# Kernel optimization log

Measured on AMD Instinct MI355X. Metric: run time of the kernel, lower is better.

Reference implementation:

```python
import jax, jax.numpy as jnp
import numpy as np

N_RES = 2_000_000
N_DOM = 2
B_WIN = 100
S_STRIDE = 10
HIDDEN = 128


def _build_windows():
    # Faithful port of the __init__ index construction.
    nb_per_res = B_WIN // S_STRIDE
    balance = B_WIN - S_STRIDE + 1
    start = np.maximum(np.arange(N_RES) + balance - B_WIN, 0)
    start = start // S_STRIDE + (start % S_STRIDE != 0).astype(np.int64)
    bs = start[:, None] + np.arange(nb_per_res)[None, :]
    return bs.astype(np.int32)


def setup_inputs() -> dict:
    key = jax.random.key(0)
    ks = jax.random.split(key, 7)
    bs_per_res = _build_windows()
    nb_windows = int(bs_per_res[-1, -1]) + 1  # 200009
    # weights near 1 (original inits to ones) so products stay well-scaled
    weights = jax.random.uniform(ks[0], (nb_windows, N_DOM), minval=0.5, maxval=1.5, dtype=jnp.float32)
    latent_variables = jax.random.normal(ks[1], (6,), dtype=jnp.float32)
    features = jax.random.normal(ks[2], (2, 50), dtype=jnp.float32)  # replaces torch.randn((2,50))
    W1 = jax.random.normal(ks[3], (53, HIDDEN), dtype=jnp.float32) * 0.1
    b1 = jnp.zeros((HIDDEN,), dtype=jnp.float32)
    W2 = jax.random.normal(ks[4], (HIDDEN, 3), dtype=jnp.float32) * 0.1
    b2 = jnp.zeros((3,), dtype=jnp.float32)
    local_frame = jax.random.normal(ks[5], (3, 3), dtype=jnp.float32)
    atom_absolute_positions = jax.random.normal(ks[6], (3 * N_RES, 3), dtype=jnp.float32)
    return {
        'weights': weights,
        'latent_variables': latent_variables,
        'features': features,
        'W1': W1, 'b1': b1, 'W2': W2, 'b2': b2,
        'local_frame': local_frame,
        'atom_absolute_positions': atom_absolute_positions,
        'bs_per_res': jnp.asarray(bs_per_res),
    }


def multiply_windows_weights(weights, bs_per_res):
    # gather: (N_res, nb_per_res, N_dom); product over the window axis, softmax over domains
    gathered = weights[bs_per_res]
    weights_per_residue = jnp.prod(gathered, axis=1)
    return jax.nn.softmax(weights_per_residue, axis=1)


def reference(weights, latent_variables, features, W1, b1, W2, b2,
              local_frame, atom_absolute_positions, bs_per_res):
    attn = multiply_windows_weights(weights, bs_per_res)  # (N_res, N_dom)
    # features_and_latent: (2, 53)
    fl = jnp.concatenate([features, latent_variables.reshape(2, 3)], axis=1)
    h = jax.nn.relu(fl @ W1 + b1)
    scalars_per_domain = h @ W2 + b2  # (N_dom, 3)
    # deform_structure: note module stores local_frame transposed
    translation_vectors = scalars_per_domain @ local_frame.T  # (N_dom, 3)
    translation_per_residue = attn @ translation_vectors      # (N_res, 3)
    new_atom_positions = atom_absolute_positions + jnp.repeat(translation_per_residue, 3, axis=0)
    return new_atom_positions, attn, translation_per_residue
```

## Files before the change

kernel.cpp:

```cpp
#include <hip/hip_runtime.h>

#define N_RES   2000000
#define HIDDEN  128

__global__ void mlp_kernel(const float* __restrict__ latent,
                           const float* __restrict__ features,
                           const float* __restrict__ W1,
                           const float* __restrict__ b1,
                           const float* __restrict__ W2,
                           const float* __restrict__ b2,
                           const float* __restrict__ lf,
                           float* __restrict__ tv_out)
{
    __shared__ float h[2][HIDDEN];
    __shared__ float s[2][3];
    const int tid = threadIdx.x;
    const int d = tid >> 7;
    const int j = tid & 127;

    float acc = b1[j];
    #pragma unroll 10
    for (int k = 0; k < 50; ++k)
        acc += features[d * 50 + k] * W1[k * HIDDEN + j];
    #pragma unroll
    for (int k = 0; k < 3; ++k)
        acc += latent[d * 3 + k] * W1[(50 + k) * HIDDEN + j];
    h[d][j] = fmaxf(acc, 0.0f);
    __syncthreads();

    if (tid < 6) {
        const int dd = tid / 3, c = tid % 3;
        float a = b2[c];
        #pragma unroll 16
        for (int k = 0; k < HIDDEN; ++k)
            a += h[dd][k] * W2[k * 3 + c];
        s[dd][c] = a;
    }
    __syncthreads();

    if (tid < 6) {
        const int dd = tid / 3, c = tid % 3;
        float a = 0.0f;
        #pragma unroll
        for (int k = 0; k < 3; ++k)
            a += s[dd][k] * lf[c * 3 + k];
        tv_out[dd * 3 + c] = a;
    }
}

__global__ void deform_kernel(const float* __restrict__ weights,
                              const float* __restrict__ pos,
                              const float* __restrict__ tv,
                              float* __restrict__ out_pos,
                              float* __restrict__ out_attn,
                              float* __restrict__ out_trans)
{
    const int r = blockIdx.x * blockDim.x + threadIdx.x;
    if (r >= N_RES) return;

    const int raw   = max(r - 9, 0);
    const int start = (raw + 9) / 10;

    const float2* wbase = (const float2*)(weights) + start;
    float p0 = 1.0f, p1 = 1.0f;
    #pragma unroll
    for (int j = 0; j < 10; ++j) {
        const float2 w = wbase[j];
        p0 *= w.x;
        p1 *= w.y;
    }

    const float m  = fmaxf(p0, p1);
    const float e0 = __expf(p0 - m);
    const float e1 = __expf(p1 - m);
    const float inv = 1.0f / (e0 + e1);
    const float a0 = e0 * inv;
    const float a1 = e1 * inv;

    ((float2*)out_attn)[r] = make_float2(a0, a1);

    const float t0 = a0 * tv[0] + a1 * tv[3];
    const float t1 = a0 * tv[1] + a1 * tv[4];
    const float t2 = a0 * tv[2] + a1 * tv[5];

    out_trans[3 * r + 0] = t0;
    out_trans[3 * r + 1] = t1;
    out_trans[3 * r + 2] = t2;

    const float* p = pos     + 9ll * r;
    float*       o = out_pos + 9ll * r;
    #pragma unroll
    for (int a = 0; a < 3; ++a) {
        o[3 * a + 0] = p[3 * a + 0] + t0;
        o[3 * a + 1] = p[3 * a + 1] + t1;
        o[3 * a + 2] = p[3 * a + 2] + t2;
    }
}

extern "C" void kernel_launch(void* const* d_in, const int* in_sizes, int n_in,
                              void* d_out, int out_size, void* d_ws, size_t ws_size,
                              hipStream_t stream) {
    const float* weights  = (const float*)d_in[0];
    const float* latent   = (const float*)d_in[1];
    const float* features = (const float*)d_in[2];
    const float* W1       = (const float*)d_in[3];
    const float* b1       = (const float*)d_in[4];
    const float* W2       = (const float*)d_in[5];
    const float* b2       = (const float*)d_in[6];
    const float* lf       = (const float*)d_in[7];
    const float* pos      = (const float*)d_in[8];

    float* out = (float*)d_out;
    float* tv  = (float*)d_ws;

    mlp_kernel<<<1, 256, 0, stream>>>(latent, features, W1, b1, W2, b2, lf, tv);

    const int blocks = (N_RES + 255) / 256;
    deform_kernel<<<blocks, 256, 0, stream>>>(
        weights, pos, tv,
        out,
        out + 18000000,
        out + 22000000);
}
```

Before: 233.7 us.

## Fuse MLP into deform kernel and coalesce position/translation I/O via LDS

Every block now recomputes the tiny MLP redundantly, which removes the separate single-block launch and the dependency between the two kernels. Position loads and stores, and the translation stores, are rewritten as block-cooperative float4 accesses, with per-residue translations staged in LDS, replacing the strided 9-float and 3-float per-thread accesses. The position loads are issued before the MLP so their latency overlaps it. In exchange, every block repeats the MLP's W1 reads and compute and adds several barriers.

```diff
diff --git a/kernel.cpp b/kernel.cpp
--- a/kernel.cpp
+++ b/kernel.cpp
@@ -2,99 +2,130 @@
 
 #define N_RES   2000000
 #define HIDDEN  128
+#define BLK     256
 
-__global__ void mlp_kernel(const float* __restrict__ latent,
-                           const float* __restrict__ features,
-                           const float* __restrict__ W1,
-                           const float* __restrict__ b1,
-                           const float* __restrict__ W2,
-                           const float* __restrict__ b2,
-                           const float* __restrict__ lf,
-                           float* __restrict__ tv_out)
+__global__ __launch_bounds__(BLK, 4) void fused_kernel(
+    const float* __restrict__ weights,
+    const float* __restrict__ latent,
+    const float* __restrict__ features,
+    const float* __restrict__ W1,
+    const float* __restrict__ b1,
+    const float* __restrict__ W2,
+    const float* __restrict__ b2,
+    const float* __restrict__ lf,
+    const float* __restrict__ pos,
+    float* __restrict__ out_pos,
+    float* __restrict__ out_attn,
+    float* __restrict__ out_trans)
 {
     __shared__ float h[2][HIDDEN];
-    __shared__ float s[2][3];
-    const int tid = threadIdx.x;
-    const int d = tid >> 7;
-    const int j = tid & 127;
+    __shared__ float sv[6];
+    __shared__ float tvs[6];
+    __shared__ __align__(16) float t_lds[3 * BLK];
 
-    float acc = b1[j];
-    #pragma unroll 10
-    for (int k = 0; k < 50; ++k)
-        acc += features[d * 50 + k] * W1[k * HIDDEN + j];
-    #pragma unroll
-    for (int k = 0; k < 3; ++k)
-        acc += latent[d * 3 + k] * W1[(50 + k) * HIDDEN + j];
-    h[d][j] = fmaxf(acc, 0.0f);
+    const int tid  = threadIdx.x;
+    const int r0   = blockIdx.x * BLK;
+    const int r    = r0 + tid;
+    const int nres = min(BLK, N_RES - r0);
+    const int nch  = (9 * nres) >> 2;
+
+    const float4* __restrict__ pos4 = (const float4*)(pos + 9ll * r0);
+    float4 pA = make_float4(0.f,0.f,0.f,0.f);
+    float4 pB = pA, pC = pA;
+    if (tid            < nch) pA = pos4[tid];
+    if (tid +     BLK  < nch) pB = pos4[tid + BLK];
+    if (tid + 2 * BLK  < nch) pC = pos4[tid + 2 * BLK];
+
+    {
+        const int d = tid >> 7, j = tid & 127;
+        float acc = b1[j];
+        #pragma unroll
+        for (int k = 0; k < 50; ++k)
+            acc += features[d * 50 + k] * W1[k * HIDDEN + j];
+        #pragma unroll
+        for (int k = 0; k < 3; ++k)
+            acc += latent[d * 3 + k] * W1[(50 + k) * HIDDEN + j];
+        h[d][j] = fmaxf(acc, 0.0f);
+    }
     __syncthreads();
-
+    {
+        const int dd   = tid >> 7;
+        const int rest = tid & 127;
+        const int c    = rest >> 5;
+        const int l    = rest & 31;
+        if (c < 3) {
+            float a = 0.f;
+            #pragma unroll
+            for (int m = 0; m < 4; ++m)
+                a += h[dd][l + 32 * m] * W2[(l + 32 * m) * 3 + c];
+            #pragma unroll
+            for (int off = 16; off >= 1; off >>= 1)
+                a += __shfl_xor(a, off, 64);
+            if (l == 0) sv[dd * 3 + c] = a + b2[c];
+        }
+    }
+    __syncthreads();
     if (tid < 6) {
         const int dd = tid / 3, c = tid % 3;
-        float a = b2[c];
-        #pragma unroll 16
-        for (int k = 0; k < HIDDEN; ++k)
-            a += h[dd][k] * W2[k * 3 + c];
-        s[dd][c] = a;
+        float a = 0.f;
+        #pragma unroll
+        for (int k = 0; k < 3; ++k)
+            a += sv[dd * 3 + k] * lf[c * 3 + k];
+        tvs[tid] = a;
     }
     __syncthreads();
 
-    if (tid < 6) {
-        const int dd = tid / 3, c = tid % 3;
-        float a = 0.0f;
+    float t0 = 0.f, t1 = 0.f, t2 = 0.f;
+    if (r < N_RES) {
+        const int raw   = max(r - 9, 0);
+        const int start = (raw + 9) / 10;
+        const float2* wbase = (const float2*)(weights) + start;
+        float p0 = 1.0f, p1 = 1.0f;
         #pragma unroll
-        for (int k = 0; k < 3; ++k)
-            a += s[dd][k] * lf[c * 3 + k];
-        tv_out[dd * 3 + c] = a;
+        for (int j = 0; j < 10; ++j) {
+            const float2 w = wbase[j];
+            p0 *= w.x;
+            p1 *= w.y;
+        }
+        const float m   = fmaxf(p0, p1);
+        const float e0  = __expf(p0 - m);
+        const float e1  = __expf(p1 - m);
+        const float inv = 1.0f / (e0 + e1);
+        const float a0  = e0 * inv;
+        const float a1  = e1 * inv;
+
+        ((float2*)out_attn)[r] = make_float2(a0, a1);
+
+        t0 = a0 * tvs[0] + a1 * tvs[3];
+        t1 = a0 * tvs[1] + a1 * tvs[4];
+        t2 = a0 * tvs[2] + a1 * tvs[5];
     }
-}
+    t_lds[3 * tid + 0] = t0;
+    t_lds[3 * tid + 1] = t1;
+    t_lds[3 * tid + 2] = t2;
+    __syncthreads();
 
-__global__ void deform_kernel(const float* __restrict__ weights,
-                              const float* __restrict__ pos,
-                              const float* __restrict__ tv,
-                              float* __restrict__ out_pos,
-                              float* __restrict__ out_attn,
-                              float* __restrict__ out_trans)
-{
-    const int r = blockIdx.x * blockDim.x + threadIdx.x;
-    if (r >= N_RES) return;
+    const int ntr = (3 * nres) >> 2;
+    if (tid < ntr)
+        ((float4*)(out_trans + 3ll * r0))[tid] = ((const float4*)t_lds)[tid];
 
-    const int raw   = max(r - 9, 0);
-    const int start = (raw + 9) / 10;
-
-    const float2* wbase = (const float2*)(weights) + start;
-    float p0 = 1.0f, p1 = 1.0f;
-    #pragma unroll
-    for (int j = 0; j < 10; ++j) {
-        const float2 w = wbase[j];
-        p0 *= w.x;
-        p1 *= w.y;
-    }
-
-    const float m  = fmaxf(p0, p1);
-    const float e0 = __expf(p0 - m);
-    const float e1 = __expf(p1 - m);
-    const float inv = 1.0f / (e0 + e1);
-    const float a0 = e0 * inv;
-    const float a1 = e1 * inv;
-
-    ((float2*)out_attn)[r] = make_float2(a0, a1);
-
-    const float t0 = a0 * tv[0] + a1 * tv[3];
-    const float t1 = a0 * tv[1] + a1 * tv[4];
-    const float t2 = a0 * tv[2] + a1 * tv[5];
-
-    out_trans[3 * r + 0] = t0;
-    out_trans[3 * r + 1] = t1;
-    out_trans[3 * r + 2] = t2;
-
-    const float* p = pos     + 9ll * r;
-    float*       o = out_pos + 9ll * r;
-    #pragma unroll
-    for (int a = 0; a < 3; ++a) {
-        o[3 * a + 0] = p[3 * a + 0] + t0;
-        o[3 * a + 1] = p[3 * a + 1] + t1;
-        o[3 * a + 2] = p[3 * a + 2] + t2;
-    }
+    float4* __restrict__ o4 = (float4*)(out_pos + 9ll * r0);
+    auto addt = [&](float4 v, int c) -> float4 {
+        float* vp = (float*)&v;
+        const int e = 4 * c;
+        #pragma unroll
+        for (int k = 0; k < 4; ++k) {
+            const int idx = e + k;
+            const int rl  = idx / 9;
+            int cm = idx - 9 * rl;
+            cm = (cm >= 6) ? cm - 6 : ((cm >= 3) ? cm - 3 : cm);
+            vp[k] += t_lds[3 * rl + cm];
+        }
+        return v;
+    };
+    if (tid            < nch) o4[tid          ] = addt(pA, tid          );
+    if (tid +     BLK  < nch) o4[tid +     BLK] = addt(pB, tid +     BLK);
+    if (tid + 2 * BLK  < nch) o4[tid + 2 * BLK] = addt(pC, tid + 2 * BLK);
 }
 
 extern "C" void kernel_launch(void* const* d_in, const int* in_sizes, int n_in,
@@ -111,13 +142,10 @@
     const float* pos      = (const float*)d_in[8];
 
     float* out = (float*)d_out;
-    float* tv  = (float*)d_ws;
 
-    mlp_kernel<<<1, 256, 0, stream>>>(latent, features, W1, b1, W2, b2, lf, tv);
-
-    const int blocks = (N_RES + 255) / 256;
-    deform_kernel<<<blocks, 256, 0, stream>>>(
-        weights, pos, tv,
+    const int blocks = (N_RES + BLK - 1) / BLK;
+    fused_kernel<<<blocks, BLK, 0, stream>>>(
+        weights, latent, features, W1, b1, W2, b2, lf, pos,
         out,
         out + 18000000,
         out + 22000000);
```

Result: slower. 247.5 us (+5.9%).
